# Kernel tuning notes

Hardware: AMD Instinct MI355X
Metric: run time of the kernel (lower is better)

The kernel has to match this reference:

```python
import jax, jax.numpy as jnp
import numpy as np

BS = 128
E4M3_MAX = 448.0
E5M2_MAX = 57344.0


def qdq(x, fmax, dt):
    # block-wise (128-wide, last dim) fp8 quantize + dequantize (simulates act_quant + dequant in fp8_gemm)
    *lead, K = x.shape
    xb = x.reshape(*lead, K // BS, BS)
    s = jnp.maximum(jnp.max(jnp.abs(xb), axis=-1, keepdims=True) / fmax, 1e-12)
    xq = (xb / s).astype(dt).astype(jnp.float32)
    return (xq * s).reshape(*lead, K)


def fp8_linear(x, w, w_scale, fmax, dt, bias=None):
    # weight is fp8-valued (stored as f32 of the rounded values) with per-output-row-block scales
    x_dq = qdq(x, fmax, dt)
    sv = jnp.repeat(w_scale, BS)[: w.shape[0]]
    y = jnp.einsum('btk,ok->bto', x_dq, w * sv[:, None])
    return y if bias is None else y + bias


def fp8_ln(x, g, gs, b, bsc, eps=1e-5):
    mean = jnp.mean(x, axis=-1, keepdims=True)
    var = jnp.mean(jnp.square(x - mean), axis=-1, keepdims=True)  # unbiased=False
    xn = (x - mean) / jnp.sqrt(var + eps)
    d = x.shape[-1]
    return xn * (g * jnp.repeat(gs, BS)[:d]) + (b * jnp.repeat(bsc, BS)[:d])


def _fwd(x, attn_mask, wq, qs, wk, ks, wv, vs, wo, os_, fc1_w, fc1_s, fc1_b, fc2_w, fc2_s, fc2_b,
         ln1_g, ln1_gs, ln1_b, ln1_bs, ln2_g, ln2_gs, ln2_b, ln2_bs):
    B, T, C = x.shape
    H = 16
    HD = C // H
    e5 = jnp.float8_e5m2
    # attention (q/k/v/out projections use E5M2 fp8)
    q = fp8_linear(x, wq, qs, E5M2_MAX, e5).reshape(B, T, H, HD).transpose(0, 2, 1, 3)
    k = fp8_linear(x, wk, ks, E5M2_MAX, e5).reshape(B, T, H, HD).transpose(0, 2, 1, 3)
    v = fp8_linear(x, wv, vs, E5M2_MAX, e5).reshape(B, T, H, HD).transpose(0, 2, 1, 3)
    scores = jnp.einsum('bhqd,bhkd->bhqk', q, k) / jnp.sqrt(jnp.float32(HD))
    scores = jnp.where(attn_mask[:, None] == 0, -jnp.inf, scores)
    attn = jax.nn.softmax(scores, axis=-1)  # dropout = identity (eval)
    ctx = jnp.einsum('bhqk,bhkd->bhqd', attn, v).transpose(0, 2, 1, 3).reshape(B, T, C)
    attn_out = fp8_linear(ctx, wo, os_, E5M2_MAX, e5)
    x = fp8_ln(x + attn_out, ln1_g, ln1_gs, ln1_b, ln1_bs)
    # MLP (E4M3 fp8)
    e4 = jnp.float8_e4m3fn
    h = fp8_linear(x, fc1_w, fc1_s, E4M3_MAX, e4, fc1_b)
    h = jax.nn.gelu(h, approximate=False)  # torch nn.GELU default = exact erf
    ffn = fp8_linear(h, fc2_w, fc2_s, E4M3_MAX, e4, fc2_b)
    x = fp8_ln(x + ffn, ln2_g, ln2_gs, ln2_b, ln2_bs)
    return x


def _xavier_fp8(key, out_f, in_f, dt):
    bound = float(np.sqrt(6.0 / (in_f + out_f)))
    w = jax.random.uniform(key, (out_f, in_f), jnp.float32, -bound, bound)
    return w.astype(dt).astype(jnp.float32)  # simulate fp8 storage


def setup_inputs() -> dict:
    key = jax.random.key(0)
    kk = jax.random.split(key, 8)
    B, T, C, MLP = 2, 1024, 2048, 8192
    e5, e4 = jnp.float8_e5m2, jnp.float8_e4m3fn
    x = jax.random.normal(kk[0], (B, T, C), jnp.float32)
    attn_mask = jnp.broadcast_to(jnp.tril(jnp.ones((T, T), jnp.int32))[None], (B, T, T))
    nb = C // BS  # 16
    inp = {
        'x': x,
        'attn_mask': attn_mask,
        'wq': _xavier_fp8(kk[1], C, C, e5), 'qs': jnp.ones(nb, jnp.float32),
        'wk': _xavier_fp8(kk[2], C, C, e5), 'ks': jnp.ones(nb, jnp.float32),
        'wv': _xavier_fp8(kk[3], C, C, e5), 'vs': jnp.ones(nb, jnp.float32),
        'wo': _xavier_fp8(kk[4], C, C, e5), 'os_': jnp.ones(nb, jnp.float32),
        'fc1_w': _xavier_fp8(kk[5], MLP, C, e4), 'fc1_s': jnp.ones(MLP // BS, jnp.float32), 'fc1_b': jnp.zeros(MLP, jnp.float32),
        'fc2_w': _xavier_fp8(kk[6], C, MLP, e4), 'fc2_s': jnp.ones(nb, jnp.float32), 'fc2_b': jnp.zeros(C, jnp.float32),
        'ln1_g': jnp.ones(C, jnp.float32), 'ln1_gs': jnp.ones(nb, jnp.float32),
        'ln1_b': jnp.zeros(C, jnp.float32), 'ln1_bs': jnp.ones(nb, jnp.float32),
        'ln2_g': jnp.ones(C, jnp.float32), 'ln2_gs': jnp.ones(nb, jnp.float32),
        'ln2_b': jnp.zeros(C, jnp.float32), 'ln2_bs': jnp.ones(nb, jnp.float32),
    }
    return inp


def reference(x, attn_mask, wq, qs, wk, ks, wv, vs, wo, os_, fc1_w, fc1_s, fc1_b, fc2_w, fc2_s, fc2_b,
              ln1_g, ln1_gs, ln1_b, ln1_bs, ln2_g, ln2_gs, ln2_b, ln2_bs):
    return _fwd(x, attn_mask, wq, qs, wk, ks, wv, vs, wo, os_, fc1_w, fc1_s, fc1_b, fc2_w, fc2_s, fc2_b,
                ln1_g, ln1_gs, ln1_b, ln1_bs, ln2_g, ln2_gs, ln2_b, ln2_bs)
```

## Files before the change

kernel.cpp:

```cpp
#include <hip/hip_runtime.h>
#include <cstdint>


typedef __bf16 bf16x8 __attribute__((ext_vector_type(8)));
typedef unsigned short u16x8 __attribute__((ext_vector_type(8)));
typedef float f32x4 __attribute__((ext_vector_type(4)));
typedef float f32x16 __attribute__((ext_vector_type(16)));
typedef int i32x8 __attribute__((ext_vector_type(8)));
typedef unsigned short u16;

#if __has_builtin(__builtin_amdgcn_exp2f)
#define EXP2F(x) __builtin_amdgcn_exp2f(x)
#else
#define EXP2F(x) exp2f(x)
#endif

__device__ __forceinline__ void gl_lds16(const void* g, void* l) {
  __builtin_amdgcn_global_load_lds(
      (const __attribute__((address_space(1))) void*)g,
      (__attribute__((address_space(3))) void*)l, 16, 0, 0);
}

struct u4x2 { uint4 a, b; };
__device__ __forceinline__ i32x8 pack8(uint4 lo, uint4 hi) {
  u4x2 t{lo, hi};
  return __builtin_bit_cast(i32x8, t);
}

__device__ __forceinline__ u16 bf16_rne(float v) {
  uint32_t u = __float_as_uint(v);
  u += 0x7FFFu + ((u >> 16) & 1u);
  return (u16)(u >> 16);
}

__device__ __forceinline__ float fp8_round(float v, int mbits, float minnorm, float subq) {
  float av = fabsf(v);
  if (av < minnorm) {
    return rintf(v / subq) * subq;
  }
  uint32_t u = __float_as_uint(v);
  const int shift = 23 - mbits;
  const uint32_t mask = (1u << shift) - 1u;
  const uint32_t rem = u & mask;
  uint32_t base = u & ~mask;
  const uint32_t half = 1u << (shift - 1);
  if (rem > half || (rem == half && ((base >> shift) & 1u))) base += (1u << shift);
  return __uint_as_float(base);
}

__device__ __forceinline__ uint8_t fp8_encode(float v, int mbits, int bias) {
  uint32_t u = __float_as_uint(v);
  uint32_t sign = (u >> 31) << 7;
  if ((u & 0x7FFFFFFFu) == 0) return (uint8_t)sign;
  int e = (int)((u >> 23) & 255u) - 127;
  if (e >= 1 - bias) {
    uint32_t mant = (u >> (23 - mbits)) & ((1u << mbits) - 1u);
    return (uint8_t)(sign | ((uint32_t)(e + bias) << mbits) | mant);
  }
  float q = fabsf(v) * __uint_as_float((uint32_t)(127 + bias - 1 + mbits) << 23);
  return (uint8_t)(sign | (uint32_t)q);
}

__global__ __launch_bounds__(256) void qdq_kernel(
    const float* __restrict__ x, uint8_t* __restrict__ q, float* __restrict__ sT,
    int nblk, int kbshift, float fmax, float minnorm, float subq, int mbits, int bias) {
  const int wid = blockIdx.x * 4 + (threadIdx.x >> 6);
  if (wid >= nblk) return;
  const int lane = threadIdx.x & 63;
  const size_t base = (size_t)wid * 128 + (size_t)lane * 2;
  float2 v = *(const float2*)(x + base);
  float am = fmaxf(fabsf(v.x), fabsf(v.y));
#pragma unroll
  for (int m = 32; m >= 1; m >>= 1) am = fmaxf(am, __shfl_xor(am, m));
  const float sc = fmaxf(am / fmax, 1e-12f);
  const float q0 = fp8_round(v.x / sc, mbits, minnorm, subq);
  const float q1 = fp8_round(v.y / sc, mbits, minnorm, subq);
  uchar2 o;
  o.x = fp8_encode(q0, mbits, bias);
  o.y = fp8_encode(q1, mbits, bias);
  *(uchar2*)(q + base) = o;
  if (lane == 0) {
    const int kbs = 1 << kbshift;
    const int m = wid >> kbshift;
    const int kb = wid & (kbs - 1);
    sT[(size_t)kb * (nblk >> kbshift) + m] = sc;
  }
}

__global__ __launch_bounds__(256) void w_to_fp8_kernel(
    const float* __restrict__ in, uint8_t* __restrict__ out, int n4, int mbits, int bias) {
  const int i = blockIdx.x * 256 + threadIdx.x;
  if (i >= n4) return;
  float4 v = ((const float4*)in)[i];
  uchar4 o;
  o.x = fp8_encode(v.x, mbits, bias);
  o.y = fp8_encode(v.y, mbits, bias);
  o.z = fp8_encode(v.z, mbits, bias);
  o.w = fp8_encode(v.w, mbits, bias);
  *(uchar4*)(out + (size_t)i * 4) = o;
}

__global__ void concat3_kernel(const float* __restrict__ a, const float* __restrict__ b,
                               const float* __restrict__ c, float* __restrict__ o, int n) {
  const int i = threadIdx.x;
  if (i < n) { o[i] = a[i]; o[n + i] = b[i]; o[2 * n + i] = c[i]; }
}

__global__ __launch_bounds__(256) void split_bf16_kernel(
    const float* __restrict__ in, u16* __restrict__ hi, u16* __restrict__ lo, int n4) {
  const int i = blockIdx.x * 256 + threadIdx.x;
  if (i >= n4) return;
  float4 v = ((const float4*)in)[i];
  float f[4] = {v.x, v.y, v.z, v.w};
  ushort4 oh, ol;
  u16* ph = (u16*)&oh;
  u16* pl = (u16*)&ol;
#pragma unroll
  for (int j = 0; j < 4; ++j) {
    u16 h = bf16_rne(f[j]);
    float hf = __uint_as_float((uint32_t)h << 16);
    ph[j] = h;
    pl[j] = bf16_rne(f[j] - hf);
  }
  ((ushort4*)hi)[i] = oh;
  ((ushort4*)lo)[i] = ol;
}

__global__ __launch_bounds__(256) void vtrans_kernel(
    const float* __restrict__ v, u16* __restrict__ vth, u16* __restrict__ vtl) {
  __shared__ float tile[64][65];
  const int tid = threadIdx.x;
  const int t0 = blockIdx.x * 64;
  const int d0 = blockIdx.y * 64;
  const int bh = blockIdx.z;
  const int b = bh >> 4, h = bh & 15;
#pragma unroll
  for (int s = 0; s < 4; ++s) {
    const int e = s * 256 + tid;
    const int r = e >> 4, c4 = e & 15;
    float4 val = *(const float4*)(v + ((size_t)(b * 1024 + t0 + r)) * 2048 + h * 128 + d0 + c4 * 4);
    tile[r][c4 * 4 + 0] = val.x;
    tile[r][c4 * 4 + 1] = val.y;
    tile[r][c4 * 4 + 2] = val.z;
    tile[r][c4 * 4 + 3] = val.w;
  }
  __syncthreads();
#pragma unroll
  for (int s = 0; s < 4; ++s) {
    const int e = s * 256 + tid;
    const int dr = e >> 4, tc4 = e & 15;
    ushort4 oh, ol;
    u16* ph = (u16*)&oh;
    u16* pl = (u16*)&ol;
#pragma unroll
    for (int i = 0; i < 4; ++i) {
      float f = tile[tc4 * 4 + i][dr];
      u16 hv = bf16_rne(f);
      ph[i] = hv;
      pl[i] = bf16_rne(f - __uint_as_float((uint32_t)hv << 16));
    }
    const size_t ob = ((size_t)(bh * 128 + d0 + dr)) * 1024 + t0 + tc4 * 4;
    *(ushort4*)(vth + ob) = oh;
    *(ushort4*)(vtl + ob) = ol;
  }
}

__global__ __launch_bounds__(256, 2) void attn_wave_kernel(
    const float* __restrict__ Q, const u16* __restrict__ Kh, const u16* __restrict__ Kl,
    const u16* __restrict__ Vth, const u16* __restrict__ Vtl, float* __restrict__ Octx) {
  constexpr int PLD = 34;
  __shared__ uint32_t Psm[4][32 * PLD];
  __shared__ float Osum[32 * 128];
  __shared__ float lsh[4][32];

  const int tid = threadIdx.x;
  const int w = tid >> 6;
  const int lane = tid & 63;
  const int l31 = lane & 31;
  const int q2 = lane >> 5;
  const int bh = blockIdx.x;
  const int b = bh >> 4;
  const int hofs = (bh & 15) * 128;
  const int qt = 31 - (int)blockIdx.y;
  const int i0 = qt * 32;
  const float SC2 = 0.12752698f;

  bf16x8 qh[8], ql[8];
  {
    const float* qp = Q + ((size_t)(b * 1024 + i0 + l31)) * 2048 + hofs + q2 * 8;
#pragma unroll
    for (int c = 0; c < 8; ++c) {
      float4 v0 = *(const float4*)(qp + c * 16);
      float4 v1 = *(const float4*)(qp + c * 16 + 4);
      float f[8] = {v0.x, v0.y, v0.z, v0.w, v1.x, v1.y, v1.z, v1.w};
      u16x8 uh, ul;
#pragma unroll
      for (int j = 0; j < 8; ++j) {
        u16 hv = bf16_rne(f[j]);
        uh[j] = hv;
        ul[j] = bf16_rne(f[j] - __uint_as_float((uint32_t)hv << 16));
      }
      qh[c] = __builtin_bit_cast(bf16x8, uh);
      ql[c] = __builtin_bit_cast(bf16x8, ul);
    }
  }

  const f32x16 z16 = {0.f};
  f32x16 Oacc[4] = {z16, z16, z16, z16};
  float lr[16];
#pragma unroll
  for (int r = 0; r < 16; ++r) lr[r] = 0.f;
  int rowq[16];
#pragma unroll
  for (int r = 0; r < 16; ++r) rowq[r] = (r & 3) + 8 * (r >> 2) + 4 * q2;

  uint32_t* Pw = Psm[w];
  for (int kt = w; kt <= qt; kt += 4) {
    const int j0 = kt * 32;
    const size_t krow = ((size_t)(b * 1024 + j0 + l31)) * 2048 + hofs + q2 * 8;
    f32x16 S = z16;
#pragma unroll
    for (int c = 0; c < 8; ++c) {
      bf16x8 k8h = *(const bf16x8*)(Kh + krow + c * 16);
      bf16x8 k8l = *(const bf16x8*)(Kl + krow + c * 16);
      S = __builtin_amdgcn_mfma_f32_32x32x16_bf16(qh[c], k8h, S, 0, 0, 0);
      S = __builtin_amdgcn_mfma_f32_32x32x16_bf16(qh[c], k8l, S, 0, 0, 0);
      S = __builtin_amdgcn_mfma_f32_32x32x16_bf16(ql[c], k8h, S, 0, 0, 0);
    }
    if (kt == qt) {
#pragma unroll
      for (int r = 0; r < 16; ++r)
        if (l31 > rowq[r]) S[r] = -3e38f;
    }
#pragma unroll
    for (int r = 0; r < 16; ++r) {
      const float p = EXP2F(S[r] * SC2);
      lr[r] += p;
      const u16 ph = bf16_rne(p);
      const u16 pl = bf16_rne(p - __uint_as_float((uint32_t)ph << 16));
      Pw[rowq[r] * PLD + l31] = (uint32_t)ph | ((uint32_t)pl << 16);
    }
#pragma unroll
    for (int s = 0; s < 2; ++s) {
      const uint32_t* rp = Pw + l31 * PLD + s * 16 + q2 * 8;
      uint2 a0 = *(const uint2*)(rp + 0);
      uint2 a1 = *(const uint2*)(rp + 2);
      uint2 a2 = *(const uint2*)(rp + 4);
      uint2 a3 = *(const uint2*)(rp + 6);
      u16x8 uh, ul;
      uh[0] = (u16)a0.x; ul[0] = (u16)(a0.x >> 16);
      uh[1] = (u16)a0.y; ul[1] = (u16)(a0.y >> 16);
      uh[2] = (u16)a1.x; ul[2] = (u16)(a1.x >> 16);
      uh[3] = (u16)a1.y; ul[3] = (u16)(a1.y >> 16);
      uh[4] = (u16)a2.x; ul[4] = (u16)(a2.x >> 16);
      uh[5] = (u16)a2.y; ul[5] = (u16)(a2.y >> 16);
      uh[6] = (u16)a3.x; ul[6] = (u16)(a3.x >> 16);
      uh[7] = (u16)a3.y; ul[7] = (u16)(a3.y >> 16);
      bf16x8 p8h = __builtin_bit_cast(bf16x8, uh);
      bf16x8 p8l = __builtin_bit_cast(bf16x8, ul);
      const size_t vrow = ((size_t)(bh * 128 + l31)) * 1024 + j0 + s * 16 + q2 * 8;
#pragma unroll
      for (int dt = 0; dt < 4; ++dt) {
        bf16x8 v8h = *(const bf16x8*)(Vth + vrow + (size_t)dt * 32768);
        bf16x8 v8l = *(const bf16x8*)(Vtl + vrow + (size_t)dt * 32768);
        Oacc[dt] = __builtin_amdgcn_mfma_f32_32x32x16_bf16(p8h, v8h, Oacc[dt], 0, 0, 0);
        Oacc[dt] = __builtin_amdgcn_mfma_f32_32x32x16_bf16(p8h, v8l, Oacc[dt], 0, 0, 0);
        Oacc[dt] = __builtin_amdgcn_mfma_f32_32x32x16_bf16(p8l, v8h, Oacc[dt], 0, 0, 0);
      }
    }
  }

#pragma unroll
  for (int r = 0; r < 16; ++r) {
    float t = lr[r];
    t += __shfl_xor(t, 1);
    t += __shfl_xor(t, 2);
    t += __shfl_xor(t, 4);
    t += __shfl_xor(t, 8);
    t += __shfl_xor(t, 16);
    lr[r] = t;
  }
  if (l31 == 0) {
#pragma unroll
    for (int r = 0; r < 16; ++r) lsh[w][rowq[r]] = lr[r];
  }
  if (w == 0) {
#pragma unroll
    for (int dt = 0; dt < 4; ++dt)
#pragma unroll
      for (int r = 0; r < 16; ++r) Osum[rowq[r] * 128 + dt * 32 + l31] = Oacc[dt][r];
  }
  __syncthreads();
  if (w == 1) {
#pragma unroll
    for (int dt = 0; dt < 4; ++dt)
#pragma unroll
      for (int r = 0; r < 16; ++r) Osum[rowq[r] * 128 + dt * 32 + l31] += Oacc[dt][r];
  }
  __syncthreads();
  if (w == 2) {
#pragma unroll
    for (int dt = 0; dt < 4; ++dt)
#pragma unroll
      for (int r = 0; r < 16; ++r) Osum[rowq[r] * 128 + dt * 32 + l31] += Oacc[dt][r];
  }
  __syncthreads();
  if (w == 3) {
#pragma unroll
    for (int dt = 0; dt < 4; ++dt)
#pragma unroll
      for (int r = 0; r < 16; ++r) Osum[rowq[r] * 128 + dt * 32 + l31] += Oacc[dt][r];
  }
  __syncthreads();
  const int row = w * 8 + (lane >> 3);
  const int c0 = (lane & 7) * 16;
  const float inv = 1.0f / (lsh[0][row] + lsh[1][row] + lsh[2][row] + lsh[3][row]);
  float* op = Octx + ((size_t)(b * 1024 + i0 + row)) * 2048 + hofs + c0;
#pragma unroll
  for (int i2 = 0; i2 < 4; ++i2) {
    float4 v = *(const float4*)(Osum + row * 128 + c0 + i2 * 4);
    v.x *= inv; v.y *= inv; v.z *= inv; v.w *= inv;
    *(float4*)(op + i2 * 4) = v;
  }
}

template <int FMT>
__global__ __launch_bounds__(256, 2) void gemm_fp8_kernel(
    const uint8_t* __restrict__ A, const float* __restrict__ sxT,
    const uint8_t* __restrict__ W, const float* __restrict__ wsc,
    const float* __restrict__ bias, float* __restrict__ out,
    int M, int N, int K, int gelu, int seg_shift, int Nw) {
  __shared__ uint8_t As[128 * 128];
  __shared__ uint8_t Ws[128 * 128];
  const int tid = threadIdx.x;
  const int lane = tid & 63;
  const int wave = tid >> 6;
  const int wm = (wave >> 1) * 64;
  const int wn = (wave & 1) * 64;
  const int l31 = lane & 31;
  const int q2 = lane >> 5;
  const int bm = blockIdx.y * 128;
  const int bn = blockIdx.x * 128;

  const int srow = wave * 8 + (lane >> 3);
  const int gchunk = (lane & 7) ^ (lane >> 3);
  const uint8_t* ga = A + (size_t)(bm + srow) * K + gchunk * 16;
  const uint8_t* gw = W + (size_t)(bn + srow) * K + gchunk * 16;
  uint8_t* la = As + srow * 128 + (lane & 7) * 16;
  uint8_t* lw = Ws + srow * 128 + (lane & 7) * 16;

  const f32x16 z16 = {0.f};
  f32x16 acc[2][2] = {{z16, z16}, {z16, z16}};

  const int nk = K >> 7;
  for (int kt = 0; kt < nk; ++kt) {
    __syncthreads();
#pragma unroll
    for (int s = 0; s < 4; ++s) {
      gl_lds16(ga + (size_t)s * 32 * K, la + s * 4096);
      gl_lds16(gw + (size_t)s * 32 * K, lw + s * 4096);
    }
    ga += 128;
    gw += 128;
    __syncthreads();
    f32x16 chk[2][2] = {{z16, z16}, {z16, z16}};
#pragma unroll
    for (int mf = 0; mf < 2; ++mf) {
      i32x8 af[2], bf2[2];
      const int c = mf * 4 + q2 * 2;
#pragma unroll
      for (int i = 0; i < 2; ++i) {
        const int r = wm + i * 32 + l31;
        const uint8_t* Ar = As + r * 128;
        const int s7 = r & 7;
        af[i] = pack8(*(const uint4*)(Ar + ((c ^ s7) * 16)),
                      *(const uint4*)(Ar + (((c + 1) ^ s7) * 16)));
      }
#pragma unroll
      for (int j = 0; j < 2; ++j) {
        const int r = wn + j * 32 + l31;
        const uint8_t* Wr = Ws + r * 128;
        const int s7 = r & 7;
        bf2[j] = pack8(*(const uint4*)(Wr + ((c ^ s7) * 16)),
                       *(const uint4*)(Wr + (((c + 1) ^ s7) * 16)));
      }
#pragma unroll
      for (int i = 0; i < 2; ++i)
#pragma unroll
        for (int j = 0; j < 2; ++j)
          chk[i][j] = __builtin_amdgcn_mfma_scale_f32_32x32x64_f8f6f4(
              af[i], bf2[j], chk[i][j], FMT, FMT, 0, 0x7F7F7F7F, 0, 0x7F7F7F7F);
    }
#pragma unroll
    for (int i = 0; i < 2; ++i) {
#pragma unroll
      for (int rg = 0; rg < 4; ++rg) {
        const f32x4 sv = *(const f32x4*)(sxT + (size_t)kt * M + bm + wm + i * 32 + rg * 8 + q2 * 4);
#pragma unroll
        for (int j = 0; j < 2; ++j)
#pragma unroll
          for (int rr = 0; rr < 4; ++rr)
            acc[i][j][rg * 4 + rr] += sv[rr] * chk[i][j][rg * 4 + rr];
      }
    }
  }
#pragma unroll
  for (int i = 0; i < 2; ++i) {
#pragma unroll
    for (int j = 0; j < 2; ++j) {
      const int n = bn + wn + j * 32 + l31;
      const float wsn = wsc[n >> 7];
      const float bv = bias ? bias[n] : 0.f;
      const int seg = n >> seg_shift;
      const int col = n & ((1 << seg_shift) - 1);
      float* op = out + (size_t)seg * M * Nw + col;
#pragma unroll
      for (int reg = 0; reg < 16; ++reg) {
        const int m = bm + wm + i * 32 + (reg & 3) + 8 * (reg >> 2) + 4 * q2;
        float v = acc[i][j][reg] * wsn + bv;
        if (gelu) v = 0.5f * v * (1.f + erff(v * 0.70710678118654752440f));
        op[(size_t)m * Nw] = v;
      }
    }
  }
}

__global__ __launch_bounds__(256) void ln_kernel(
    const float* __restrict__ a, const float* __restrict__ b2,
    const float* __restrict__ g, const float* __restrict__ gs,
    const float* __restrict__ bb, const float* __restrict__ bs,
    float* __restrict__ out, int C) {
  __shared__ float red[4];
  const int tid = threadIdx.x;
  const int row = blockIdx.x;
  const float* pa = a + (size_t)row * C;
  const float* pb = b2 + (size_t)row * C;
  float v[8];
  float sum = 0.f;
#pragma unroll
  for (int k = 0; k < 8; ++k) {
    const int c = tid + (k << 8);
    v[k] = pa[c] + pb[c];
    sum += v[k];
  }
#pragma unroll
  for (int m = 32; m >= 1; m >>= 1) sum += __shfl_xor(sum, m);
  if ((tid & 63) == 0) red[tid >> 6] = sum;
  __syncthreads();
  const float mean = (red[0] + red[1] + red[2] + red[3]) * (1.f / 2048.f);
  __syncthreads();
  float sq = 0.f;
#pragma unroll
  for (int k = 0; k < 8; ++k) {
    const float d = v[k] - mean;
    sq += d * d;
  }
#pragma unroll
  for (int m = 32; m >= 1; m >>= 1) sq += __shfl_xor(sq, m);
  if ((tid & 63) == 0) red[tid >> 6] = sq;
  __syncthreads();
  const float var = (red[0] + red[1] + red[2] + red[3]) * (1.f / 2048.f);
  const float inv = 1.0f / sqrtf(var + 1e-5f);
  float* po = out + (size_t)row * C;
#pragma unroll
  for (int k = 0; k < 8; ++k) {
    const int c = tid + (k << 8);
    po[c] = (v[k] - mean) * inv * (g[c] * gs[c >> 7]) + bb[c] * bs[c >> 7];
  }
}

extern "C" void kernel_launch(void* const* d_in, const int* in_sizes, int n_in,
                              void* d_out, int out_size, void* d_ws, size_t ws_size,
                              hipStream_t stream) {
  const int C = 2048, MLP = 8192;
  const int M = 2048;

  const float* x = (const float*)d_in[0];
  const float* wq = (const float*)d_in[2];
  const float* qs = (const float*)d_in[3];
  const float* wk = (const float*)d_in[4];
  const float* ks = (const float*)d_in[5];
  const float* wv = (const float*)d_in[6];
  const float* vs = (const float*)d_in[7];
  const float* wo = (const float*)d_in[8];
  const float* os_ = (const float*)d_in[9];
  const float* fc1_w = (const float*)d_in[10];
  const float* fc1_s = (const float*)d_in[11];
  const float* fc1_b = (const float*)d_in[12];
  const float* fc2_w = (const float*)d_in[13];
  const float* fc2_s = (const float*)d_in[14];
  const float* fc2_b = (const float*)d_in[15];
  const float* ln1_g = (const float*)d_in[16];
  const float* ln1_gs = (const float*)d_in[17];
  const float* ln1_b = (const float*)d_in[18];
  const float* ln1_bs = (const float*)d_in[19];
  const float* ln2_g = (const float*)d_in[20];
  const float* ln2_gs = (const float*)d_in[21];
  const float* ln2_b = (const float*)d_in[22];
  const float* ln2_bs = (const float*)d_in[23];

  char* ws = (char*)d_ws;
  const size_t o_Aq = 0;
  const size_t o_Wb = 33554432;
  const size_t o_sx = 67108864;
  const size_t o_ln1 = 67633152;
  const size_t o_q = 84410368;
  const size_t o_k = 101187584;
  const size_t o_v = 117964800;
  const size_t o_ctx = 134742016;
  const size_t o_attn = 151519232;
  const size_t o_h = o_q;
  const size_t o_ffn = o_attn;
  if (ws_size < 168296448ull) return;

  uint8_t* Aq = (uint8_t*)(ws + o_Aq);
  uint8_t* Wb = (uint8_t*)(ws + o_Wb);
  float* sx = (float*)(ws + o_sx);
  float* wsc3 = (float*)(ws + o_sx + 262144);
  float* ln1o = (float*)(ws + o_ln1);
  float* qb = (float*)(ws + o_q);
  float* kb = (float*)(ws + o_k);
  float* vb = (float*)(ws + o_v);
  float* ctx = (float*)(ws + o_ctx);
  float* attn_out = (float*)(ws + o_attn);
  float* hb = (float*)(ws + o_h);
  float* ffn = (float*)(ws + o_ffn);
  float* outp = (float*)d_out;
  u16* Kh = (u16*)(ws + o_Aq);
  u16* Kl = (u16*)(ws + o_Aq + 8388608);
  u16* Vth = (u16*)(ws + o_Aq + 16777216);
  u16* Vtl = (u16*)(ws + o_Aq + 25165824);

  const float E5_MAX = 57344.f, E5_MINN = 6.103515625e-05f, E5_SUBQ = 1.52587890625e-05f;
  const float E4_MAX = 448.f, E4_MINN = 0.015625f, E4_SUBQ = 0.001953125f;

  const dim3 blk(256);
  const int wc_qkv = (C * C / 4 + 255) / 256;
  const int wc_fc = (C * MLP / 4 + 255) / 256;

  qdq_kernel<<<M * (C / 128) / 4, blk, 0, stream>>>(x, Aq, sx, M * (C / 128), 4, E5_MAX, E5_MINN, E5_SUBQ, 2, 15);
  w_to_fp8_kernel<<<wc_qkv, blk, 0, stream>>>(wq, Wb, C * C / 4, 2, 15);
  w_to_fp8_kernel<<<wc_qkv, blk, 0, stream>>>(wk, Wb + C * C, C * C / 4, 2, 15);
  w_to_fp8_kernel<<<wc_qkv, blk, 0, stream>>>(wv, Wb + 2 * C * C, C * C / 4, 2, 15);
  concat3_kernel<<<1, 64, 0, stream>>>(qs, ks, vs, wsc3, C / 128);
  gemm_fp8_kernel<1><<<dim3(3 * C / 128, M / 128), blk, 0, stream>>>(
      Aq, sx, Wb, wsc3, nullptr, qb, M, 3 * C, C, 0, 11, C);

  split_bf16_kernel<<<(M * C / 4 + 255) / 256, blk, 0, stream>>>(kb, Kh, Kl, M * C / 4);
  vtrans_kernel<<<dim3(16, 2, 32), blk, 0, stream>>>(vb, Vth, Vtl);
  attn_wave_kernel<<<dim3(32, 32), blk, 0, stream>>>(qb, Kh, Kl, Vth, Vtl, ctx);

  qdq_kernel<<<M * (C / 128) / 4, blk, 0, stream>>>(ctx, Aq, sx, M * (C / 128), 4, E5_MAX, E5_MINN, E5_SUBQ, 2, 15);
  w_to_fp8_kernel<<<wc_qkv, blk, 0, stream>>>(wo, Wb, C * C / 4, 2, 15);
  gemm_fp8_kernel<1><<<dim3(C / 128, M / 128), blk, 0, stream>>>(
      Aq, sx, Wb, os_, nullptr, attn_out, M, C, C, 0, 30, C);

  ln_kernel<<<M, blk, 0, stream>>>(x, attn_out, ln1_g, ln1_gs, ln1_b, ln1_bs, ln1o, C);

  qdq_kernel<<<M * (C / 128) / 4, blk, 0, stream>>>(ln1o, Aq, sx, M * (C / 128), 4, E4_MAX, E4_MINN, E4_SUBQ, 3, 7);
  w_to_fp8_kernel<<<wc_fc, blk, 0, stream>>>(fc1_w, Wb, C * MLP / 4, 3, 7);
  gemm_fp8_kernel<0><<<dim3(MLP / 128, M / 128), blk, 0, stream>>>(
      Aq, sx, Wb, fc1_s, fc1_b, hb, M, MLP, C, 1, 30, MLP);

  qdq_kernel<<<M * (MLP / 128) / 4, blk, 0, stream>>>(hb, Aq, sx, M * (MLP / 128), 6, E4_MAX, E4_MINN, E4_SUBQ, 3, 7);
  w_to_fp8_kernel<<<wc_fc, blk, 0, stream>>>(fc2_w, Wb, C * MLP / 4, 3, 7);
  gemm_fp8_kernel<0><<<dim3(C / 128, M / 128), blk, 0, stream>>>(
      Aq, sx, Wb, fc2_s, fc2_b, ffn, M, C, MLP, 0, 30, C);

  ln_kernel<<<M, blk, 0, stream>>>(ln1o, ffn, ln2_g, ln2_gs, ln2_b, ln2_bs, outp, C);
}
```

Before: 654.3 us.

## Double-buffer LDS tiles in fp8 GEMM and swizzle workgroup order

The fp8 GEMM now double-buffers its A/W tiles in LDS. The global-to-LDS load for the next K tile is issued before the MFMAs on the current tile, which cuts the two barriers per iteration to one and overlaps memory traffic with compute. Block IDs are also remapped in groups of 8 to change which tiles run concurrently, likely for cache locality across XCDs. The per-row activation scales are now loaded before the MFMAs. This doubles LDS use to 64KB per block, which may reduce occupancy against the launch bound of 2. The unrolled loop by two also assumes an even number of K tiles, and the remap assumes the block count divides by 8.

```diff
diff --git a/kernel.cpp b/kernel.cpp
--- a/kernel.cpp
+++ b/kernel.cpp
@@ -330,8 +330,8 @@
     const uint8_t* __restrict__ W, const float* __restrict__ wsc,
     const float* __restrict__ bias, float* __restrict__ out,
     int M, int N, int K, int gelu, int seg_shift, int Nw) {
-  __shared__ uint8_t As[128 * 128];
-  __shared__ uint8_t Ws[128 * 128];
+  __shared__ uint8_t As[2][128 * 128];
+  __shared__ uint8_t Ws[2][128 * 128];
   const int tid = threadIdx.x;
   const int lane = tid & 63;
   const int wave = tid >> 6;
@@ -339,30 +339,50 @@
   const int wn = (wave & 1) * 64;
   const int l31 = lane & 31;
   const int q2 = lane >> 5;
-  const int bm = blockIdx.y * 128;
-  const int bn = blockIdx.x * 128;
+
+  const int gx = gridDim.x;
+  const int nwg = gx * (int)gridDim.y;
+  int id = (int)blockIdx.y * gx + (int)blockIdx.x;
+  id = (id & 7) * (nwg >> 3) + (id >> 3);
+  const int bn = (id % gx) * 128;
+  const int bm = (id / gx) * 128;
 
   const int srow = wave * 8 + (lane >> 3);
   const int gchunk = (lane & 7) ^ (lane >> 3);
   const uint8_t* ga = A + (size_t)(bm + srow) * K + gchunk * 16;
   const uint8_t* gw = W + (size_t)(bn + srow) * K + gchunk * 16;
-  uint8_t* la = As + srow * 128 + (lane & 7) * 16;
-  uint8_t* lw = Ws + srow * 128 + (lane & 7) * 16;
+  const int lofs = srow * 128 + (lane & 7) * 16;
+  const float* sxp = sxT + bm + wm + q2 * 4;
 
   const f32x16 z16 = {0.f};
   f32x16 acc[2][2] = {{z16, z16}, {z16, z16}};
 
-  const int nk = K >> 7;
-  for (int kt = 0; kt < nk; ++kt) {
-    __syncthreads();
-#pragma unroll
-    for (int s = 0; s < 4; ++s) {
-      gl_lds16(ga + (size_t)s * 32 * K, la + s * 4096);
-      gl_lds16(gw + (size_t)s * 32 * K, lw + s * 4096);
-    }
-    ga += 128;
-    gw += 128;
-    __syncthreads();
+#pragma unroll
+  for (int s = 0; s < 4; ++s) {
+    gl_lds16(ga + (size_t)s * 32 * K, &As[0][lofs + s * 4096]);
+    gl_lds16(gw + (size_t)s * 32 * K, &Ws[0][lofs + s * 4096]);
+  }
+  ga += 128;
+  gw += 128;
+  __syncthreads();
+
+  auto do_tile = [&](const uint8_t* Asc, const uint8_t* Wsc,
+                     uint8_t* Asn, uint8_t* Wsn, int kt, bool stage) {
+    if (stage) {
+#pragma unroll
+      for (int s = 0; s < 4; ++s) {
+        gl_lds16(ga + (size_t)s * 32 * K, Asn + s * 4096);
+        gl_lds16(gw + (size_t)s * 32 * K, Wsn + s * 4096);
+      }
+      ga += 128;
+      gw += 128;
+    }
+    f32x4 sv[2][4];
+#pragma unroll
+    for (int i = 0; i < 2; ++i)
+#pragma unroll
+      for (int rg = 0; rg < 4; ++rg)
+        sv[i][rg] = *(const f32x4*)(sxp + (size_t)kt * M + i * 32 + rg * 8);
     f32x16 chk[2][2] = {{z16, z16}, {z16, z16}};
 #pragma unroll
     for (int mf = 0; mf < 2; ++mf) {
@@ -371,7 +391,7 @@
 #pragma unroll
       for (int i = 0; i < 2; ++i) {
         const int r = wm + i * 32 + l31;
-        const uint8_t* Ar = As + r * 128;
+        const uint8_t* Ar = Asc + r * 128;
         const int s7 = r & 7;
         af[i] = pack8(*(const uint4*)(Ar + ((c ^ s7) * 16)),
                       *(const uint4*)(Ar + (((c + 1) ^ s7) * 16)));
@@ -379,7 +399,7 @@
 #pragma unroll
       for (int j = 0; j < 2; ++j) {
         const int r = wn + j * 32 + l31;
-        const uint8_t* Wr = Ws + r * 128;
+        const uint8_t* Wr = Wsc + r * 128;
         const int s7 = r & 7;
         bf2[j] = pack8(*(const uint4*)(Wr + ((c ^ s7) * 16)),
                        *(const uint4*)(Wr + (((c + 1) ^ s7) * 16)));
@@ -392,18 +412,23 @@
               af[i], bf2[j], chk[i][j], FMT, FMT, 0, 0x7F7F7F7F, 0, 0x7F7F7F7F);
     }
 #pragma unroll
-    for (int i = 0; i < 2; ++i) {
-#pragma unroll
-      for (int rg = 0; rg < 4; ++rg) {
-        const f32x4 sv = *(const f32x4*)(sxT + (size_t)kt * M + bm + wm + i * 32 + rg * 8 + q2 * 4);
+    for (int i = 0; i < 2; ++i)
+#pragma unroll
+      for (int rg = 0; rg < 4; ++rg)
 #pragma unroll
         for (int j = 0; j < 2; ++j)
 #pragma unroll
           for (int rr = 0; rr < 4; ++rr)
-            acc[i][j][rg * 4 + rr] += sv[rr] * chk[i][j][rg * 4 + rr];
-      }
-    }
-  }
+            acc[i][j][rg * 4 + rr] += sv[i][rg][rr] * chk[i][j][rg * 4 + rr];
+    __syncthreads();
+  };
+
+  const int nk = K >> 7;
+  for (int kt = 0; kt < nk; kt += 2) {
+    do_tile(As[0], Ws[0], &As[1][lofs], &Ws[1][lofs], kt, true);
+    do_tile(As[1], Ws[1], &As[0][lofs], &Ws[0][lofs], kt + 1, kt + 2 < nk);
+  }
+
 #pragma unroll
   for (int i = 0; i < 2; ++i) {
 #pragma unroll
```

New measurement: 684.9 us. 1.05x slower.

## Double-buffer fp8 GEMM LDS tiles and preload activation scales into shared memory

Applied to the files above, without the earlier changes.

Changes the fp8 GEMM main loop from single-buffered LDS loads with two barriers per k-step to a two-stage ping-pong pipeline. The next tile's global-to-LDS loads are issued while the current tile is being consumed, with explicit vmcnt waits. Per-row activation scales for the whole K range are preloaded into shared memory up front instead of being read from global memory every iteration. This doubles LDS tile usage and adds scale storage, and it lowers the occupancy hint to 1 block per CU for the K=8192 (NK=64) GEMM, so latency hiding now depends on the pipeline rather than on multiple resident blocks.

```diff
diff --git a/kernel.cpp b/kernel.cpp
--- a/kernel.cpp
+++ b/kernel.cpp
@@ -14,6 +14,8 @@
 #else
 #define EXP2F(x) exp2f(x)
 #endif
+
+#define CFENCE() asm volatile("" ::: "memory")
 
 __device__ __forceinline__ void gl_lds16(const void* g, void* l) {
   __builtin_amdgcn_global_load_lds(
@@ -324,14 +326,16 @@
   }
 }
 
-template <int FMT>
-__global__ __launch_bounds__(256, 2) void gemm_fp8_kernel(
+template <int FMT, int NK>
+__global__ __launch_bounds__(256, (NK <= 16 ? 2 : 1)) void gemm_fp8_kernel(
     const uint8_t* __restrict__ A, const float* __restrict__ sxT,
     const uint8_t* __restrict__ W, const float* __restrict__ wsc,
     const float* __restrict__ bias, float* __restrict__ out,
     int M, int N, int K, int gelu, int seg_shift, int Nw) {
-  __shared__ uint8_t As[128 * 128];
-  __shared__ uint8_t Ws[128 * 128];
+  __shared__ uint8_t As[2][16384];
+  __shared__ uint8_t Ws[2][16384];
+  __shared__ float sxs[NK * 128];
+
   const int tid = threadIdx.x;
   const int lane = tid & 63;
   const int wave = tid >> 6;
@@ -342,27 +346,46 @@
   const int bm = blockIdx.y * 128;
   const int bn = blockIdx.x * 128;
 
+#pragma unroll
+  for (int t = 0; t < NK * 128 / 1024; ++t) {
+    const int e = t * 1024 + tid * 4;
+    const int kt = e >> 7, r = e & 127;
+    *(float4*)(sxs + e) = *(const float4*)(sxT + (size_t)kt * M + bm + r);
+  }
+  asm volatile("s_waitcnt vmcnt(0) lgkmcnt(0)" ::: "memory");
+  __builtin_amdgcn_s_barrier();
+  CFENCE();
+
   const int srow = wave * 8 + (lane >> 3);
   const int gchunk = (lane & 7) ^ (lane >> 3);
   const uint8_t* ga = A + (size_t)(bm + srow) * K + gchunk * 16;
   const uint8_t* gw = W + (size_t)(bn + srow) * K + gchunk * 16;
-  uint8_t* la = As + srow * 128 + (lane & 7) * 16;
-  uint8_t* lw = Ws + srow * 128 + (lane & 7) * 16;
+  const int lofs = srow * 128 + (lane & 7) * 16;
 
   const f32x16 z16 = {0.f};
   f32x16 acc[2][2] = {{z16, z16}, {z16, z16}};
 
-  const int nk = K >> 7;
-  for (int kt = 0; kt < nk; ++kt) {
-    __syncthreads();
-#pragma unroll
-    for (int s = 0; s < 4; ++s) {
-      gl_lds16(ga + (size_t)s * 32 * K, la + s * 4096);
-      gl_lds16(gw + (size_t)s * 32 * K, lw + s * 4096);
-    }
-    ga += 128;
-    gw += 128;
-    __syncthreads();
+#pragma unroll
+  for (int s = 0; s < 4; ++s) {
+    gl_lds16(ga + (size_t)s * 32 * K, &As[0][lofs + s * 4096]);
+    gl_lds16(gw + (size_t)s * 32 * K, &Ws[0][lofs + s * 4096]);
+  }
+  ga += 128;
+  gw += 128;
+#pragma unroll
+  for (int s = 0; s < 4; ++s) {
+    gl_lds16(ga + (size_t)s * 32 * K, &As[1][lofs + s * 4096]);
+    gl_lds16(gw + (size_t)s * 32 * K, &Ws[1][lofs + s * 4096]);
+  }
+  ga += 128;
+  gw += 128;
+  asm volatile("s_waitcnt vmcnt(8)" ::: "memory");
+  __builtin_amdgcn_s_barrier();
+  CFENCE();
+
+  for (int kt = 0; kt < NK; ++kt) {
+    const uint8_t* Asc = As[kt & 1];
+    const uint8_t* Wsc = Ws[kt & 1];
     f32x16 chk[2][2] = {{z16, z16}, {z16, z16}};
 #pragma unroll
     for (int mf = 0; mf < 2; ++mf) {
@@ -371,7 +394,7 @@
 #pragma unroll
       for (int i = 0; i < 2; ++i) {
         const int r = wm + i * 32 + l31;
-        const uint8_t* Ar = As + r * 128;
+        const uint8_t* Ar = Asc + r * 128;
         const int s7 = r & 7;
         af[i] = pack8(*(const uint4*)(Ar + ((c ^ s7) * 16)),
                       *(const uint4*)(Ar + (((c + 1) ^ s7) * 16)));
@@ -379,7 +402,7 @@
 #pragma unroll
       for (int j = 0; j < 2; ++j) {
         const int r = wn + j * 32 + l31;
-        const uint8_t* Wr = Ws + r * 128;
+        const uint8_t* Wr = Wsc + r * 128;
         const int s7 = r & 7;
         bf2[j] = pack8(*(const uint4*)(Wr + ((c ^ s7) * 16)),
                        *(const uint4*)(Wr + (((c + 1) ^ s7) * 16)));
@@ -391,11 +414,12 @@
           chk[i][j] = __builtin_amdgcn_mfma_scale_f32_32x32x64_f8f6f4(
               af[i], bf2[j], chk[i][j], FMT, FMT, 0, 0x7F7F7F7F, 0, 0x7F7F7F7F);
     }
+    const float* svl = sxs + kt * 128 + wm + q2 * 4;
 #pragma unroll
     for (int i = 0; i < 2; ++i) {
 #pragma unroll
       for (int rg = 0; rg < 4; ++rg) {
-        const f32x4 sv = *(const f32x4*)(sxT + (size_t)kt * M + bm + wm + i * 32 + rg * 8 + q2 * 4);
+        const f32x4 sv = *(const f32x4*)(svl + i * 32 + rg * 8);
 #pragma unroll
         for (int j = 0; j < 2; ++j)
 #pragma unroll
@@ -403,7 +427,29 @@
             acc[i][j][rg * 4 + rr] += sv[rr] * chk[i][j][rg * 4 + rr];
       }
     }
-  }
+    CFENCE();
+    __builtin_amdgcn_s_barrier();
+    CFENCE();
+    if (kt + 1 < NK) {
+      if (kt + 2 < NK) {
+        uint8_t* Asn = As[kt & 1];
+        uint8_t* Wsn = Ws[kt & 1];
+#pragma unroll
+        for (int s = 0; s < 4; ++s) {
+          gl_lds16(ga + (size_t)s * 32 * K, Asn + lofs + s * 4096);
+          gl_lds16(gw + (size_t)s * 32 * K, Wsn + lofs + s * 4096);
+        }
+        ga += 128;
+        gw += 128;
+        asm volatile("s_waitcnt vmcnt(8)" ::: "memory");
+      } else {
+        asm volatile("s_waitcnt vmcnt(0)" ::: "memory");
+      }
+      __builtin_amdgcn_s_barrier();
+      CFENCE();
+    }
+  }
+
 #pragma unroll
   for (int i = 0; i < 2; ++i) {
 #pragma unroll
@@ -543,7 +589,7 @@
   w_to_fp8_kernel<<<wc_qkv, blk, 0, stream>>>(wk, Wb + C * C, C * C / 4, 2, 15);
   w_to_fp8_kernel<<<wc_qkv, blk, 0, stream>>>(wv, Wb + 2 * C * C, C * C / 4, 2, 15);
   concat3_kernel<<<1, 64, 0, stream>>>(qs, ks, vs, wsc3, C / 128);
-  gemm_fp8_kernel<1><<<dim3(3 * C / 128, M / 128), blk, 0, stream>>>(
+  gemm_fp8_kernel<1, 16><<<dim3(3 * C / 128, M / 128), blk, 0, stream>>>(
       Aq, sx, Wb, wsc3, nullptr, qb, M, 3 * C, C, 0, 11, C);
 
   split_bf16_kernel<<<(M * C / 4 + 255) / 256, blk, 0, stream>>>(kb, Kh, Kl, M * C / 4);
@@ -552,19 +598,19 @@
 
   qdq_kernel<<<M * (C / 128) / 4, blk, 0, stream>>>(ctx, Aq, sx, M * (C / 128), 4, E5_MAX, E5_MINN, E5_SUBQ, 2, 15);
   w_to_fp8_kernel<<<wc_qkv, blk, 0, stream>>>(wo, Wb, C * C / 4, 2, 15);
-  gemm_fp8_kernel<1><<<dim3(C / 128, M / 128), blk, 0, stream>>>(
+  gemm_fp8_kernel<1, 16><<<dim3(C / 128, M / 128), blk, 0, stream>>>(
       Aq, sx, Wb, os_, nullptr, attn_out, M, C, C, 0, 30, C);
 
   ln_kernel<<<M, blk, 0, stream>>>(x, attn_out, ln1_g, ln1_gs, ln1_b, ln1_bs, ln1o, C);
 
   qdq_kernel<<<M * (C / 128) / 4, blk, 0, stream>>>(ln1o, Aq, sx, M * (C / 128), 4, E4_MAX, E4_MINN, E4_SUBQ, 3, 7);
   w_to_fp8_kernel<<<wc_fc, blk, 0, stream>>>(fc1_w, Wb, C * MLP / 4, 3, 7);
-  gemm_fp8_kernel<0><<<dim3(MLP / 128, M / 128), blk, 0, stream>>>(
+  gemm_fp8_kernel<0, 16><<<dim3(MLP / 128, M / 128), blk, 0, stream>>>(
       Aq, sx, Wb, fc1_s, fc1_b, hb, M, MLP, C, 1, 30, MLP);
 
   qdq_kernel<<<M * (MLP / 128) / 4, blk, 0, stream>>>(hb, Aq, sx, M * (MLP / 128), 6, E4_MAX, E4_MINN, E4_SUBQ, 3, 7);
   w_to_fp8_kernel<<<wc_fc, blk, 0, stream>>>(fc2_w, Wb, C * MLP / 4, 3, 7);
-  gemm_fp8_kernel<0><<<dim3(C / 128, M / 128), blk, 0, stream>>>(
+  gemm_fp8_kernel<0, 64><<<dim3(C / 128, M / 128), blk, 0, stream>>>(
       Aq, sx, Wb, fc2_s, fc2_b, ffn, M, C, MLP, 0, 30, C);
 
   ln_kernel<<<M, blk, 0, stream>>>(ln1o, ffn, ln2_g, ln2_gs, ln2_b, ln2_bs, outp, C);
```

After: 701.7 us. +7.2%, slower.

## Fuse activation fp8 quantization into attention, LN and fc1 GEMM epilogues

Applied to the files above, without the earlier changes.

Moves the block-wise fp8 quantize of the attention context, LN1 output and GELU output into the epilogues of the kernels that produce them. This removes three standalone qdq passes and the fp32 round trips of ctx and h through memory. It also merges the three QKV weight conversions into one launch and raises MFMA instruction priority in the attention loop. The fused epilogues add cross-lane reductions, an extra LDS buffer and a barrier in the GEMM, and a byte-wise scattered store of the quantized fc1 output, which may cost some of the savings.

```diff
diff --git a/kernel.cpp b/kernel.cpp
--- a/kernel.cpp
+++ b/kernel.cpp
@@ -59,6 +59,13 @@
   }
   float q = fabsf(v) * __uint_as_float((uint32_t)(127 + bias - 1 + mbits) << 23);
   return (uint8_t)(sign | (uint32_t)q);
+}
+
+__device__ __forceinline__ uint8_t q_e5(float v, float sc) {
+  return fp8_encode(fp8_round(v / sc, 2, 6.103515625e-05f, 1.52587890625e-05f), 2, 15);
+}
+__device__ __forceinline__ uint8_t q_e4(float v, float sc) {
+  return fp8_encode(fp8_round(v / sc, 3, 0.015625f, 0.001953125f), 3, 7);
 }
 
 __global__ __launch_bounds__(256) void qdq_kernel(
@@ -100,6 +107,21 @@
   *(uchar4*)(out + (size_t)i * 4) = o;
 }
 
+__global__ __launch_bounds__(256) void w3_to_fp8_kernel(
+    const float* __restrict__ a, const float* __restrict__ b,
+    const float* __restrict__ c, uint8_t* __restrict__ out, int n4) {
+  const int i = blockIdx.x * 256 + threadIdx.x;
+  if (i >= n4) return;
+  const float* in = blockIdx.y == 0 ? a : (blockIdx.y == 1 ? b : c);
+  float4 v = ((const float4*)in)[i];
+  uchar4 o;
+  o.x = fp8_encode(v.x, 2, 15);
+  o.y = fp8_encode(v.y, 2, 15);
+  o.z = fp8_encode(v.z, 2, 15);
+  o.w = fp8_encode(v.w, 2, 15);
+  *(uchar4*)(out + (size_t)blockIdx.y * n4 * 4 + (size_t)i * 4) = o;
+}
+
 __global__ void concat3_kernel(const float* __restrict__ a, const float* __restrict__ b,
                                const float* __restrict__ c, float* __restrict__ o, int n) {
   const int i = threadIdx.x;
@@ -167,7 +189,8 @@
 
 __global__ __launch_bounds__(256, 2) void attn_wave_kernel(
     const float* __restrict__ Q, const u16* __restrict__ Kh, const u16* __restrict__ Kl,
-    const u16* __restrict__ Vth, const u16* __restrict__ Vtl, float* __restrict__ Octx) {
+    const u16* __restrict__ Vth, const u16* __restrict__ Vtl,
+    uint8_t* __restrict__ Aqo, float* __restrict__ sTo) {
   constexpr int PLD = 34;
   __shared__ uint32_t Psm[4][32 * PLD];
   __shared__ float Osum[32 * 128];
@@ -223,9 +246,11 @@
     for (int c = 0; c < 8; ++c) {
       bf16x8 k8h = *(const bf16x8*)(Kh + krow + c * 16);
       bf16x8 k8l = *(const bf16x8*)(Kl + krow + c * 16);
+      __builtin_amdgcn_s_setprio(1);
       S = __builtin_amdgcn_mfma_f32_32x32x16_bf16(qh[c], k8h, S, 0, 0, 0);
       S = __builtin_amdgcn_mfma_f32_32x32x16_bf16(qh[c], k8l, S, 0, 0, 0);
       S = __builtin_amdgcn_mfma_f32_32x32x16_bf16(ql[c], k8h, S, 0, 0, 0);
+      __builtin_amdgcn_s_setprio(0);
     }
     if (kt == qt) {
 #pragma unroll
@@ -263,9 +288,11 @@
       for (int dt = 0; dt < 4; ++dt) {
         bf16x8 v8h = *(const bf16x8*)(Vth + vrow + (size_t)dt * 32768);
         bf16x8 v8l = *(const bf16x8*)(Vtl + vrow + (size_t)dt * 32768);
+        __builtin_amdgcn_s_setprio(1);
         Oacc[dt] = __builtin_amdgcn_mfma_f32_32x32x16_bf16(p8h, v8h, Oacc[dt], 0, 0, 0);
         Oacc[dt] = __builtin_amdgcn_mfma_f32_32x32x16_bf16(p8h, v8l, Oacc[dt], 0, 0, 0);
         Oacc[dt] = __builtin_amdgcn_mfma_f32_32x32x16_bf16(p8l, v8h, Oacc[dt], 0, 0, 0);
+        __builtin_amdgcn_s_setprio(0);
       }
     }
   }
@@ -315,23 +342,40 @@
   const int row = w * 8 + (lane >> 3);
   const int c0 = (lane & 7) * 16;
   const float inv = 1.0f / (lsh[0][row] + lsh[1][row] + lsh[2][row] + lsh[3][row]);
-  float* op = Octx + ((size_t)(b * 1024 + i0 + row)) * 2048 + hofs + c0;
+  float vq[16];
+  float am = 0.f;
 #pragma unroll
   for (int i2 = 0; i2 < 4; ++i2) {
     float4 v = *(const float4*)(Osum + row * 128 + c0 + i2 * 4);
-    v.x *= inv; v.y *= inv; v.z *= inv; v.w *= inv;
-    *(float4*)(op + i2 * 4) = v;
-  }
-}
-
-template <int FMT>
-__global__ __launch_bounds__(256, 2) void gemm_fp8_kernel(
+    vq[i2 * 4 + 0] = v.x * inv;
+    vq[i2 * 4 + 1] = v.y * inv;
+    vq[i2 * 4 + 2] = v.z * inv;
+    vq[i2 * 4 + 3] = v.w * inv;
+  }
+#pragma unroll
+  for (int t = 0; t < 16; ++t) am = fmaxf(am, fabsf(vq[t]));
+  am = fmaxf(am, __shfl_xor(am, 1));
+  am = fmaxf(am, __shfl_xor(am, 2));
+  am = fmaxf(am, __shfl_xor(am, 4));
+  const float sc = fmaxf(am / 57344.f, 1e-12f);
+  uint8_t qb8[16];
+#pragma unroll
+  for (int t = 0; t < 16; ++t) qb8[t] = q_e5(vq[t], sc);
+  const int token = b * 1024 + i0 + row;
+  *(uint4*)(Aqo + (size_t)token * 2048 + hofs + c0) = *(const uint4*)qb8;
+  if ((lane & 7) == 0) sTo[(size_t)(bh & 15) * 2048 + token] = sc;
+}
+
+template <int FMT, int QOUT>
+__global__ __launch_bounds__(256, 2) void gemm_simple(
     const uint8_t* __restrict__ A, const float* __restrict__ sxT,
     const uint8_t* __restrict__ W, const float* __restrict__ wsc,
     const float* __restrict__ bias, float* __restrict__ out,
+    uint8_t* __restrict__ outq, float* __restrict__ sTq,
     int M, int N, int K, int gelu, int seg_shift, int Nw) {
   __shared__ uint8_t As[128 * 128];
   __shared__ uint8_t Ws[128 * 128];
+  __shared__ float rowred[2][128];
   const int tid = threadIdx.x;
   const int lane = tid & 63;
   const int wave = tid >> 6;
@@ -404,6 +448,59 @@
       }
     }
   }
+
+  if (QOUT) {
+#pragma unroll
+    for (int i = 0; i < 2; ++i) {
+#pragma unroll
+      for (int j = 0; j < 2; ++j) {
+        const int n = bn + wn + j * 32 + l31;
+        const float wsn = wsc[n >> 7];
+        const float bv = bias[n];
+#pragma unroll
+        for (int reg = 0; reg < 16; ++reg) {
+          float v = acc[i][j][reg] * wsn + bv;
+          acc[i][j][reg] = 0.5f * v * (1.f + erff(v * 0.70710678118654752440f));
+        }
+      }
+    }
+#pragma unroll
+    for (int i = 0; i < 2; ++i) {
+      float am2[16];
+#pragma unroll
+      for (int reg = 0; reg < 16; ++reg)
+        am2[reg] = fmaxf(fabsf(acc[i][0][reg]), fabsf(acc[i][1][reg]));
+#pragma unroll
+      for (int reg = 0; reg < 16; ++reg) {
+        am2[reg] = fmaxf(am2[reg], __shfl_xor(am2[reg], 1));
+        am2[reg] = fmaxf(am2[reg], __shfl_xor(am2[reg], 2));
+        am2[reg] = fmaxf(am2[reg], __shfl_xor(am2[reg], 4));
+        am2[reg] = fmaxf(am2[reg], __shfl_xor(am2[reg], 8));
+        am2[reg] = fmaxf(am2[reg], __shfl_xor(am2[reg], 16));
+      }
+      if (l31 == 0) {
+#pragma unroll
+        for (int reg = 0; reg < 16; ++reg)
+          rowred[wave & 1][wm + i * 32 + (reg & 3) + 8 * (reg >> 2) + 4 * q2] = am2[reg];
+      }
+    }
+    __syncthreads();
+#pragma unroll
+    for (int i = 0; i < 2; ++i) {
+#pragma unroll
+      for (int reg = 0; reg < 16; ++reg) {
+        const int rloc = wm + i * 32 + (reg & 3) + 8 * (reg >> 2) + 4 * q2;
+        const float sc = fmaxf(fmaxf(rowred[0][rloc], rowred[1][rloc]) / 448.f, 1e-12f);
+        const int m = bm + rloc;
+#pragma unroll
+        for (int j = 0; j < 2; ++j)
+          outq[(size_t)m * N + bn + wn + j * 32 + l31] = q_e4(acc[i][j][reg], sc);
+        if ((wave & 1) == 0 && l31 == 0) sTq[(size_t)(bn >> 7) * M + m] = sc;
+      }
+    }
+    return;
+  }
+
 #pragma unroll
   for (int i = 0; i < 2; ++i) {
 #pragma unroll
@@ -425,12 +522,15 @@
   }
 }
 
+template <int QOUT>
 __global__ __launch_bounds__(256) void ln_kernel(
     const float* __restrict__ a, const float* __restrict__ b2,
     const float* __restrict__ g, const float* __restrict__ gs,
     const float* __restrict__ bb, const float* __restrict__ bs,
-    float* __restrict__ out, int C) {
+    float* __restrict__ out, uint8_t* __restrict__ outq, float* __restrict__ sT,
+    int C) {
   __shared__ float red[4];
+  __shared__ float wred[8][4];
   const int tid = threadIdx.x;
   const int row = blockIdx.x;
   const float* pa = a + (size_t)row * C;
@@ -462,10 +562,36 @@
   const float var = (red[0] + red[1] + red[2] + red[3]) * (1.f / 2048.f);
   const float inv = 1.0f / sqrtf(var + 1e-5f);
   float* po = out + (size_t)row * C;
+  float o[8];
 #pragma unroll
   for (int k = 0; k < 8; ++k) {
     const int c = tid + (k << 8);
-    po[c] = (v[k] - mean) * inv * (g[c] * gs[c >> 7]) + bb[c] * bs[c >> 7];
+    o[k] = (v[k] - mean) * inv * (g[c] * gs[c >> 7]) + bb[c] * bs[c >> 7];
+    po[c] = o[k];
+  }
+  if (QOUT) {
+    const int w = tid >> 6;
+#pragma unroll
+    for (int k = 0; k < 8; ++k) {
+      float am = fabsf(o[k]);
+      am = fmaxf(am, __shfl_xor(am, 1));
+      am = fmaxf(am, __shfl_xor(am, 2));
+      am = fmaxf(am, __shfl_xor(am, 4));
+      am = fmaxf(am, __shfl_xor(am, 8));
+      am = fmaxf(am, __shfl_xor(am, 16));
+      am = fmaxf(am, __shfl_xor(am, 32));
+      if ((tid & 63) == 0) wred[k][w] = am;
+    }
+    __syncthreads();
+    const int hsel = (tid >> 7) * 2;
+#pragma unroll
+    for (int k = 0; k < 8; ++k) {
+      const float bm = fmaxf(wred[k][hsel], wred[k][hsel + 1]);
+      const float sc = fmaxf(bm / 448.f, 1e-12f);
+      const int c = tid + (k << 8);
+      outq[(size_t)row * C + c] = q_e4(o[k], sc);
+      if ((tid & 127) == 0) sT[(size_t)((k << 1) | (tid >> 7)) * 2048 + row] = sc;
+    }
   }
 }
 
@@ -509,7 +635,6 @@
   const size_t o_v = 117964800;
   const size_t o_ctx = 134742016;
   const size_t o_attn = 151519232;
-  const size_t o_h = o_q;
   const size_t o_ffn = o_attn;
   if (ws_size < 168296448ull) return;
 
@@ -521,9 +646,10 @@
   float* qb = (float*)(ws + o_q);
   float* kb = (float*)(ws + o_k);
   float* vb = (float*)(ws + o_v);
-  float* ctx = (float*)(ws + o_ctx);
+  uint8_t* Aq2 = (uint8_t*)(ws + o_ctx);
   float* attn_out = (float*)(ws + o_attn);
-  float* hb = (float*)(ws + o_h);
+  uint8_t* Aq3 = (uint8_t*)(ws + o_q);
+  float* sxk = (float*)(ws + o_k);
   float* ffn = (float*)(ws + o_ffn);
   float* outp = (float*)d_out;
   u16* Kh = (u16*)(ws + o_Aq);
@@ -539,33 +665,30 @@
   const int wc_fc = (C * MLP / 4 + 255) / 256;
 
   qdq_kernel<<<M * (C / 128) / 4, blk, 0, stream>>>(x, Aq, sx, M * (C / 128), 4, E5_MAX, E5_MINN, E5_SUBQ, 2, 15);
-  w_to_fp8_kernel<<<wc_qkv, blk, 0, stream>>>(wq, Wb, C * C / 4, 2, 15);
-  w_to_fp8_kernel<<<wc_qkv, blk, 0, stream>>>(wk, Wb + C * C, C * C / 4, 2, 15);
-  w_to_fp8_kernel<<<wc_qkv, blk, 0, stream>>>(wv, Wb + 2 * C * C, C * C / 4, 2, 15);
+  w3_to_fp8_kernel<<<dim3(wc_qkv, 3), blk, 0, stream>>>(wq, wk, wv, Wb, C * C / 4);
   concat3_kernel<<<1, 64, 0, stream>>>(qs, ks, vs, wsc3, C / 128);
-  gemm_fp8_kernel<1><<<dim3(3 * C / 128, M / 128), blk, 0, stream>>>(
-      Aq, sx, Wb, wsc3, nullptr, qb, M, 3 * C, C, 0, 11, C);
+  gemm_simple<1, 0><<<dim3(3 * C / 128, M / 128), blk, 0, stream>>>(
+      Aq, sx, Wb, wsc3, nullptr, qb, nullptr, nullptr, M, 3 * C, C, 0, 11, C);
 
   split_bf16_kernel<<<(M * C / 4 + 255) / 256, blk, 0, stream>>>(kb, Kh, Kl, M * C / 4);
   vtrans_kernel<<<dim3(16, 2, 32), blk, 0, stream>>>(vb, Vth, Vtl);
-  attn_wave_kernel<<<dim3(32, 32), blk, 0, stream>>>(qb, Kh, Kl, Vth, Vtl, ctx);
-
-  qdq_kernel<<<M * (C / 128) / 4, blk, 0, stream>>>(ctx, Aq, sx, M * (C / 128), 4, E5_MAX, E5_MINN, E5_SUBQ, 2, 15);
+  attn_wave_kernel<<<dim3(32, 32), blk, 0, stream>>>(qb, Kh, Kl, Vth, Vtl, Aq2, sx);
+
   w_to_fp8_kernel<<<wc_qkv, blk, 0, stream>>>(wo, Wb, C * C / 4, 2, 15);
-  gemm_fp8_kernel<1><<<dim3(C / 128, M / 128), blk, 0, stream>>>(
-      Aq, sx, Wb, os_, nullptr, attn_out, M, C, C, 0, 30, C);
-
-  ln_kernel<<<M, blk, 0, stream>>>(x, attn_out, ln1_g, ln1_gs, ln1_b, ln1_bs, ln1o, C);
-
-  qdq_kernel<<<M * (C / 128) / 4, blk, 0, stream>>>(ln1o, Aq, sx, M * (C / 128), 4, E4_MAX, E4_MINN, E4_SUBQ, 3, 7);
+  gemm_simple<1, 0><<<dim3(C / 128, M / 128), blk, 0, stream>>>(
+      Aq2, sx, Wb, os_, nullptr, attn_out, nullptr, nullptr, M, C, C, 0, 30, C);
+
+  ln_kernel<1><<<M, blk, 0, stream>>>(x, attn_out, ln1_g, ln1_gs, ln1_b, ln1_bs,
+                                      ln1o, Aq, sx, C);
+
   w_to_fp8_kernel<<<wc_fc, blk, 0, stream>>>(fc1_w, Wb, C * MLP / 4, 3, 7);
-  gemm_fp8_kernel<0><<<dim3(MLP / 128, M / 128), blk, 0, stream>>>(
-      Aq, sx, Wb, fc1_s, fc1_b, hb, M, MLP, C, 1, 30, MLP);
-
-  qdq_kernel<<<M * (MLP / 128) / 4, blk, 0, stream>>>(hb, Aq, sx, M * (MLP / 128), 6, E4_MAX, E4_MINN, E4_SUBQ, 3, 7);
+  gemm_simple<0, 1><<<dim3(MLP / 128, M / 128), blk, 0, stream>>>(
+      Aq, sx, Wb, fc1_s, fc1_b, nullptr, Aq3, sxk, M, MLP, C, 1, 30, MLP);
+
   w_to_fp8_kernel<<<wc_fc, blk, 0, stream>>>(fc2_w, Wb, C * MLP / 4, 3, 7);
-  gemm_fp8_kernel<0><<<dim3(C / 128, M / 128), blk, 0, stream>>>(
-      Aq, sx, Wb, fc2_s, fc2_b, ffn, M, C, MLP, 0, 30, C);
-
-  ln_kernel<<<M, blk, 0, stream>>>(ln1o, ffn, ln2_g, ln2_gs, ln2_b, ln2_bs, outp, C);
-}
+  gemm_simple<0, 0><<<dim3(C / 128, M / 128), blk, 0, stream>>>(
+      Aq3, sxk, Wb, fc2_s, fc2_b, ffn, nullptr, nullptr, M, C, MLP, 0, 30, C);
+
+  ln_kernel<0><<<M, blk, 0, stream>>>(ln1o, ffn, ln2_g, ln2_gs, ln2_b, ln2_bs,
+                                      outp, nullptr, nullptr, C);
+}
```

Result: no change. 657.2 us (+0.4%).
